# Performance work log

Measured on AMD Instinct MI355X. Metric: run time of the kernel, lower is better.

## Reference

```python
import jax, jax.numpy as jnp
import numpy as np

B, R, CIN, J, O, ITERS = 512, 1152, 8, 10, 16, 3  # batch, routes, in_ch, capsules, out_ch, routing iters


def squash(s, axis):
    # v = (||s||^2 / (1 + ||s||^2)) * s / ||s||  (standard CapsNet squash)
    sq = jnp.sum(s * s, axis=axis, keepdims=True)
    return (sq / (1.0 + sq)) * s * jax.lax.rsqrt(sq + 1e-8)


def setup_inputs() -> dict:
    key = jax.random.key(0)
    k1, k2 = jax.random.split(key)
    x = jax.random.normal(k1, (B, R, CIN), dtype=jnp.float32)
    W = jax.random.normal(k2, (R, J, O, CIN), dtype=jnp.float32)  # param, batch-broadcast
    return {"x": x, "W": W}


def reference(x, W):
    # u_hat[b,r,j,:] = W[r,j] @ x[b,r]   (replaces torch stack/cat broadcasting)
    u_hat = jnp.einsum('rjoc,brc->brjo', W, x)  # [B,R,J,O]
    b_ij = jnp.zeros((x.shape[0], R, J), dtype=x.dtype)
    v = None
    for it in range(ITERS):
        c_ij = jax.nn.softmax(b_ij, axis=2)                 # softmax over capsules j
        s_j = jnp.einsum('brj,brjo->bjo', c_ij, u_hat)      # weighted sum over routes
        v = squash(s_j, axis=-1)                            # [B,J,O]
        if it < ITERS - 1:
            b_ij = b_ij + jnp.einsum('brjo,bjo->brj', u_hat, v)  # agreement
    # torch returns v_j.squeeze(1) with shape [B, J, O, 1]
    return v[..., None]
```

## Files before the change

### kernel.cpp

```cpp
#include <hip/hip_runtime.h>
#include <hip/hip_fp16.h>
#include <cstdint>
#include <cstddef>

#define NB 512
#define NR 1152
#define NC 8
#define NJ 10
#define NO 16
#define NJO 160
#define NRC 36

typedef unsigned int uint32;

union H2U { __half2 h; uint32 u; };

__device__ __forceinline__ uint32 packf16(float a0, float a1) {
    H2U p;
    p.h = __halves2half2(__float2half_rn(a0), __float2half_rn(a1));
    return p.u;
}
__device__ __forceinline__ float2 unpackf16(uint32 w) {
    H2U p; p.u = w;
    return __half22float2(p.h);
}

__device__ __forceinline__ float dot8f(float4 p, float4 q, float4 xa, float4 xb) {
    return p.x * xa.x + p.y * xa.y + p.z * xa.z + p.w * xa.w
         + q.x * xb.x + q.y * xb.y + q.z * xb.z + q.w * xb.w;
}

__global__ __launch_bounds__(256) void xpose_kernel(const float* __restrict__ x,
                                                    float* __restrict__ xT) {
    const int r0 = blockIdx.x * 16;
    const int b0 = blockIdx.y * 64;
    const int t  = threadIdx.x;
    __shared__ float tile[16][65][8];

    for (int i = t; i < 2048; i += 256) {
        int b = i >> 5, r = (i >> 1) & 15, h = i & 1;
        float4 v = *(const float4*)&x[(size_t)(b0 + b) * (NR * NC) + (size_t)(r0 + r) * NC + h * 4];
        *(float4*)&tile[r][b][h * 4] = v;
    }
    __syncthreads();
    for (int i = t; i < 2048; i += 256) {
        int r = i >> 7, b = (i >> 1) & 63, h = i & 1;
        float4 v = *(const float4*)&tile[r][b][h * 4];
        *(float4*)&xT[(size_t)(r0 + r) * (NB * NC) + (size_t)(b0 + b) * NC + h * 4] = v;
    }
}

__global__ __launch_bounds__(320) void uhat_kernel(const float* __restrict__ xT,
                                                   const float* __restrict__ W,
                                                   uint32* __restrict__ u) {
    const int r = blockIdx.x;
    const int t = threadIdx.x;

    __shared__ float Ws[NC][NJO + 4];
    __shared__ float xs[NB][NC];

    for (int i = t; i < NJO * NC; i += 320) {
        Ws[i & 7][i >> 3] = W[(size_t)r * (NJO * NC) + i];
    }
    {
        const float4* xsrc = (const float4*)(xT + (size_t)r * (NB * NC));
        float4* xdst = (float4*)&xs[0][0];
        for (int i = t; i < (NB * NC) / 4; i += 320) xdst[i] = xsrc[i];
    }
    __syncthreads();

    const int ni   = t % 80;
    const int half = t / 80;
    const int g    = ni / 10;
    const int rem  = ni % 10;
    const int qt   = g >> 1;
    const int jh   = g & 1;
    const int j    = jh * 5 + (rem >> 1);
    const int d    = rem & 1;
    const int jo0  = 16 * j + 4 * qt + 2 * d;

    float w0[8], w1[8];
#pragma unroll
    for (int c = 0; c < 8; ++c) {
        w0[c] = Ws[c][jo0];
        w1[c] = Ws[c][jo0 + 1];
    }

    for (int b = half; b < NB; b += 4) {
        const float4* xp = (const float4*)xs[b];
        float4 xa = xp[0], xb = xp[1];
        float a0 = w0[0] * xa.x + w0[1] * xa.y + w0[2] * xa.z + w0[3] * xa.w
                 + w0[4] * xb.x + w0[5] * xb.y + w0[6] * xb.z + w0[7] * xb.w;
        float a1 = w1[0] * xa.x + w1[1] * xa.y + w1[2] * xa.z + w1[3] * xa.w
                 + w1[4] * xb.x + w1[5] * xb.y + w1[6] * xb.z + w1[7] * xb.w;
        u[(size_t)(b * NR + r) * 80 + ni] = packf16(a0, a1);
    }
}

__global__ __launch_bounds__(320) void s0gemm_kernel(const float* __restrict__ x,
                                                     const float* __restrict__ W,
                                                     float* __restrict__ s0p) {
    const int b0 = blockIdx.x * 32;
    const int rc = blockIdx.y;
    const int r0 = rc * 32;
    const int t  = threadIdx.x;

    __shared__ float xs[32][32][8];

    for (int i = t; i < 2048; i += 320) {
        int bloc = i >> 6, rloc = (i >> 1) & 31, h = i & 1;
        float4 v = *(const float4*)&x[(size_t)(b0 + bloc) * (NR * NC) + (size_t)(r0 + rloc) * NC + h * 4];
        *(float4*)&xs[rloc][bloc][h * 4] = v;
    }
    __syncthreads();

    const int jo = t % 160;
    const int bh = t / 160;

    const float* wp = W + (size_t)r0 * (NJO * NC) + (size_t)jo * NC;

    float acc[16];
#pragma unroll
    for (int i = 0; i < 16; ++i) acc[i] = 0.0f;

#pragma unroll 1
    for (int rloc = 0; rloc < 32; ++rloc) {
        const float* wr = wp + (size_t)rloc * (NJO * NC);
        float4 w0 = *(const float4*)wr;
        float4 w1 = *(const float4*)(wr + 4);
#pragma unroll
        for (int bs = 0; bs < 16; ++bs) {
            const float* xp = xs[rloc][bh * 16 + bs];
            float4 xa = *(const float4*)xp;
            float4 xb = *(const float4*)(xp + 4);
            acc[bs] += dot8f(w0, w1, xa, xb);
        }
    }

#pragma unroll
    for (int bs = 0; bs < 16; ++bs) {
        s0p[((size_t)rc * NB + (b0 + bh * 16 + bs)) * NJO + jo] = acc[bs];
    }
}

#define LOADROW(Q0, Q1, Q2, Q3, Q4, ROW)                                      \
    {                                                                         \
        const uint32* p_ = ubase + (size_t)(ROW) * 80;                        \
        Q0 = *(const uint2*)(p_);     Q1 = *(const uint2*)(p_ + 2);           \
        Q2 = *(const uint2*)(p_ + 4); Q3 = *(const uint2*)(p_ + 6);           \
        Q4 = *(const uint2*)(p_ + 8);                                         \
    }

#define PROCESS(Q0, Q1, Q2, Q3, Q4)                                           \
    {                                                                         \
        uint32 ur[10];                                                        \
        ur[0] = Q0.x; ur[1] = Q0.y; ur[2] = Q1.x; ur[3] = Q1.y;               \
        ur[4] = Q2.x; ur[5] = Q2.y; ur[6] = Q3.x; ur[7] = Q3.y;               \
        ur[8] = Q4.x; ur[9] = Q4.y;                                           \
        float cj[5];                                                          \
        {                                                                     \
            float sum = 0.0f;                                                 \
            _Pragma("unroll")                                                 \
            for (int jl = 0; jl < 5; ++jl) {                                  \
                float2 ua = unpackf16(ur[2 * jl]);                            \
                float2 ub = unpackf16(ur[2 * jl + 1]);                        \
                float4 vv = *(const float4*)&vls[vbase + 16 * jl];            \
                float pj = ua.x * vv.x + ua.y * vv.y + ub.x * vv.z + ub.y * vv.w; \
                pj += __shfl_xor(pj, 1);                                      \
                pj += __shfl_xor(pj, 2);                                      \
                float e = __expf(pj);                                         \
                cj[jl] = e;                                                   \
                sum += e;                                                     \
            }                                                                 \
            sum += __shfl_xor(sum, 4);                                        \
            float inv = 1.0f / sum;                                           \
            _Pragma("unroll")                                                 \
            for (int jl = 0; jl < 5; ++jl) cj[jl] *= inv;                     \
        }                                                                     \
        _Pragma("unroll")                                                     \
        for (int jl = 0; jl < 5; ++jl) {                                      \
            float2 ua = unpackf16(ur[2 * jl]);                                \
            float2 ub = unpackf16(ur[2 * jl + 1]);                            \
            acc[4 * jl + 0] += cj[jl] * ua.x;                                 \
            acc[4 * jl + 1] += cj[jl] * ua.y;                                 \
            acc[4 * jl + 2] += cj[jl] * ub.x;                                 \
            acc[4 * jl + 3] += cj[jl] * ub.y;                                 \
        }                                                                     \
    }

__global__ __launch_bounds__(576, 2) void routing_kernel(const uint32* __restrict__ u,
                                                         const float* __restrict__ s0p,
                                                         float* __restrict__ outp) {
    const int b    = blockIdx.x;
    const int t    = threadIdx.x;
    const int w    = t >> 6;
    const int l    = t & 63;
    const int qt   = l & 3;
    const int jh   = (l >> 2) & 1;
    const int mloc = l >> 3;
    const int g    = qt * 2 + jh;

    __shared__ float sl[NJO];
    __shared__ float vls[NJO];
    __shared__ float vaccl[NJO];

    for (int i = t; i < NJO; i += 576) sl[i] = 0.0f;

    if (t < 80) {
        float sx = 0.0f, sy = 0.0f;
#pragma unroll 6
        for (int rc = 0; rc < NRC; ++rc) {
            float2 p = *(const float2*)&s0p[((size_t)rc * NB + b) * NJO + 2 * t];
            sx += p.x; sy += p.y;
        }
        sx *= 0.1f; sy *= 0.1f;
        float sq = sx * sx + sy * sy;
#pragma unroll
        for (int off = 1; off < 8; off <<= 1) sq += __shfl_xor(sq, off, 8);
        float scale = (sq / (1.0f + sq)) * rsqrtf(sq + 1e-8f);
        float vx = sx * scale, vy = sy * scale;
        *(float2*)&vaccl[2 * t] = make_float2(vx, vy);
        *(float2*)&vls[2 * t]   = make_float2(vx, vy);
    }
    __syncthreads();

    const uint32* ubase = u + (size_t)b * (NR * 80) + g * 10;
    const int vbase = jh * 80 + qt * 4;
    const int rbase = w * 128 + mloc;

#pragma unroll 1
    for (int it = 1; it < 3; ++it) {
        float acc[20];
#pragma unroll
        for (int i = 0; i < 20; ++i) acc[i] = 0.0f;

        uint2 qa0, qa1, qa2, qa3, qa4;
        uint2 qb0, qb1, qb2, qb3, qb4;

        LOADROW(qa0, qa1, qa2, qa3, qa4, rbase)

#pragma unroll 1
        for (int c16 = 0; c16 < 16; c16 += 2) {
            LOADROW(qb0, qb1, qb2, qb3, qb4, rbase + (c16 + 1) * 8)
            PROCESS(qa0, qa1, qa2, qa3, qa4)
            if (c16 < 14) {
                LOADROW(qa0, qa1, qa2, qa3, qa4, rbase + (c16 + 2) * 8)
            }
            PROCESS(qb0, qb1, qb2, qb3, qb4)
        }

        float a[12];
        {
            const int bit = (l >> 3) & 1;
#pragma unroll
            for (int i = 0; i < 12; ++i) {
                float lo = acc[i];
                float hi = (i + 12 < 20) ? acc[i + 12] : 0.0f;
                float send = bit ? lo : hi;
                float recv = __shfl_xor(send, 8);
                a[i] = (bit ? hi : lo) + recv;
            }
        }
#pragma unroll
        for (int st = 1; st < 3; ++st) {
            const int h = 12 >> st;
            const int bit = (l >> (3 + st)) & 1;
#pragma unroll
            for (int i = 0; i < 6; ++i) {
                if (i < h) {
                    float send = bit ? a[i] : a[i + h];
                    float recv = __shfl_xor(send, 8 << st);
                    a[i] = (bit ? a[i + h] : a[i]) + recv;
                }
            }
        }
        const int base = 3 * (__brev((uint32)mloc) >> 29);
#pragma unroll
        for (int i = 0; i < 3; ++i) {
            int aidx = base + i;
            if (aidx < 20) {
                int jl = aidx >> 2, e = aidx & 3;
                atomicAdd(&sl[16 * (jh * 5 + jl) + 4 * qt + e], a[i]);
            }
        }
        __syncthreads();

        if (t < 80) {
            float2 sv = *(const float2*)&sl[2 * t];
            float sq = sv.x * sv.x + sv.y * sv.y;
#pragma unroll
            for (int off = 1; off < 8; off <<= 1) sq += __shfl_xor(sq, off, 8);
            float scale = (sq / (1.0f + sq)) * rsqrtf(sq + 1e-8f);
            float vx = sv.x * scale, vy = sv.y * scale;
            if (it == 2) {
                *(float2*)&outp[b * NJO + 2 * t] = make_float2(vx, vy);
            } else {
                float2 va = *(const float2*)&vaccl[2 * t];
                va.x += vx; va.y += vy;
                *(float2*)&vaccl[2 * t] = va;
                *(float2*)&vls[2 * t]   = va;
            }
        }
        __syncthreads();
        if (it < 2) {
            for (int i = t; i < NJO; i += 576) sl[i] = 0.0f;
            __syncthreads();
        }
    }
}

extern "C" void kernel_launch(void* const* d_in, const int* in_sizes, int n_in,
                              void* d_out, int out_size, void* d_ws, size_t ws_size,
                              hipStream_t stream) {
    (void)in_sizes; (void)n_in; (void)out_size; (void)ws_size;

    const float* x = (const float*)d_in[0];
    const float* W = (const float*)d_in[1];
    float* out = (float*)d_out;

    char* ws = (char*)d_ws;
    const size_t XBYTES = (size_t)NR * NB * NC * 4;
    float*  xT  = (float*)ws;
    uint32* u   = (uint32*)(ws + XBYTES);
    float*  s0p = (float*)ws;

    xpose_kernel<<<dim3(NR / 16, NB / 64), 256, 0, stream>>>(x, xT);
    uhat_kernel<<<NR, 320, 0, stream>>>(xT, W, u);
    s0gemm_kernel<<<dim3(16, NRC), 320, 0, stream>>>(x, W, s0p);
    routing_kernel<<<NB, 576, 0, stream>>>(u, s0p, out);
}
```

Before: 240.9 us.

## Fuse s0 GEMM into uhat kernel and add fallback three-pass routing

The s0 partial GEMM is folded into the tail of the uhat kernel: the first 576 blocks reuse their shared memory to compute s0 partials, with a retiled thread mapping that writes float4 stores. This removes one kernel launch and lets s0 work overlap uhat work, but s0p must now live in its own workspace region. When the workspace is too small, a new routing kernel computes the first routing iteration from u_hat with uniform coefficients instead of reading s0p.

```diff
diff --git a/kernel.cpp b/kernel.cpp
--- a/kernel.cpp
+++ b/kernel.cpp
@@ -52,12 +52,16 @@
 
 __global__ __launch_bounds__(320) void uhat_kernel(const float* __restrict__ xT,
                                                    const float* __restrict__ W,
-                                                   uint32* __restrict__ u) {
+                                                   uint32* __restrict__ u,
+                                                   const float* __restrict__ x,
+                                                   float* __restrict__ s0p,
+                                                   int do_s0) {
     const int r = blockIdx.x;
     const int t = threadIdx.x;
 
-    __shared__ float Ws[NC][NJO + 4];
-    __shared__ float xs[NB][NC];
+    __shared__ char shm[32768 + 512];
+    float (*Ws)[NJO + 4] = (float (*)[NJO + 4])shm;
+    float (*xs)[NC]      = (float (*)[NC])(shm + 5248);
 
     for (int i = t; i < NJO * NC; i += 320) {
         Ws[i & 7][i >> 3] = W[(size_t)r * (NJO * NC) + i];
@@ -71,75 +75,84 @@
 
     const int ni   = t % 80;
     const int half = t / 80;
-    const int g    = ni / 10;
-    const int rem  = ni % 10;
-    const int qt   = g >> 1;
-    const int jh   = g & 1;
-    const int j    = jh * 5 + (rem >> 1);
-    const int d    = rem & 1;
-    const int jo0  = 16 * j + 4 * qt + 2 * d;
-
-    float w0[8], w1[8];
-#pragma unroll
-    for (int c = 0; c < 8; ++c) {
-        w0[c] = Ws[c][jo0];
-        w1[c] = Ws[c][jo0 + 1];
-    }
-
-    for (int b = half; b < NB; b += 4) {
-        const float4* xp = (const float4*)xs[b];
-        float4 xa = xp[0], xb = xp[1];
-        float a0 = w0[0] * xa.x + w0[1] * xa.y + w0[2] * xa.z + w0[3] * xa.w
-                 + w0[4] * xb.x + w0[5] * xb.y + w0[6] * xb.z + w0[7] * xb.w;
-        float a1 = w1[0] * xa.x + w1[1] * xa.y + w1[2] * xa.z + w1[3] * xa.w
-                 + w1[4] * xb.x + w1[5] * xb.y + w1[6] * xb.z + w1[7] * xb.w;
-        u[(size_t)(b * NR + r) * 80 + ni] = packf16(a0, a1);
-    }
-}
-
-__global__ __launch_bounds__(320) void s0gemm_kernel(const float* __restrict__ x,
-                                                     const float* __restrict__ W,
-                                                     float* __restrict__ s0p) {
-    const int b0 = blockIdx.x * 32;
-    const int rc = blockIdx.y;
-    const int r0 = rc * 32;
-    const int t  = threadIdx.x;
-
-    __shared__ float xs[32][32][8];
-
-    for (int i = t; i < 2048; i += 320) {
-        int bloc = i >> 6, rloc = (i >> 1) & 31, h = i & 1;
-        float4 v = *(const float4*)&x[(size_t)(b0 + bloc) * (NR * NC) + (size_t)(r0 + rloc) * NC + h * 4];
-        *(float4*)&xs[rloc][bloc][h * 4] = v;
-    }
-    __syncthreads();
-
-    const int jo = t % 160;
-    const int bh = t / 160;
-
-    const float* wp = W + (size_t)r0 * (NJO * NC) + (size_t)jo * NC;
-
-    float acc[16];
-#pragma unroll
-    for (int i = 0; i < 16; ++i) acc[i] = 0.0f;
+    {
+        const int g    = ni / 10;
+        const int rem  = ni % 10;
+        const int qt   = g >> 1;
+        const int jh   = g & 1;
+        const int j    = jh * 5 + (rem >> 1);
+        const int d    = rem & 1;
+        const int jo0  = 16 * j + 4 * qt + 2 * d;
+
+        float w0[8], w1[8];
+#pragma unroll
+        for (int c = 0; c < 8; ++c) {
+            w0[c] = Ws[c][jo0];
+            w1[c] = Ws[c][jo0 + 1];
+        }
+
+        for (int b = half; b < NB; b += 4) {
+            const float4* xp = (const float4*)xs[b];
+            float4 xa = xp[0], xb = xp[1];
+            float a0 = w0[0] * xa.x + w0[1] * xa.y + w0[2] * xa.z + w0[3] * xa.w
+                     + w0[4] * xb.x + w0[5] * xb.y + w0[6] * xb.z + w0[7] * xb.w;
+            float a1 = w1[0] * xa.x + w1[1] * xa.y + w1[2] * xa.z + w1[3] * xa.w
+                     + w1[4] * xb.x + w1[5] * xb.y + w1[6] * xb.z + w1[7] * xb.w;
+            u[(size_t)(b * NR + r) * 80 + ni] = packf16(a0, a1);
+        }
+    }
+
+    if (do_s0 && r < 576) {
+        __syncthreads();
+        float (*xs2)[32][NC] = (float (*)[32][NC])shm;
+
+        const int b0s = (r % 16) * 32;
+        const int rc  = r / 16;
+        const int r0  = rc * 32;
+
+        for (int i = t; i < 2048; i += 320) {
+            int bloc = i >> 6, rloc = (i >> 1) & 31, h = i & 1;
+            float4 v = *(const float4*)&x[(size_t)(b0s + bloc) * (NR * NC) + (size_t)(r0 + rloc) * NC + h * 4];
+            *(float4*)&xs2[rloc][bloc][h * 4] = v;
+        }
+        __syncthreads();
+
+        const int joq = t % 40;
+        const int bq  = t / 40;
+
+        float acc[16];
+#pragma unroll
+        for (int i = 0; i < 16; ++i) acc[i] = 0.0f;
 
 #pragma unroll 1
-    for (int rloc = 0; rloc < 32; ++rloc) {
-        const float* wr = wp + (size_t)rloc * (NJO * NC);
-        float4 w0 = *(const float4*)wr;
-        float4 w1 = *(const float4*)(wr + 4);
-#pragma unroll
-        for (int bs = 0; bs < 16; ++bs) {
-            const float* xp = xs[rloc][bh * 16 + bs];
-            float4 xa = *(const float4*)xp;
-            float4 xb = *(const float4*)(xp + 4);
-            acc[bs] += dot8f(w0, w1, xa, xb);
-        }
-    }
-
-#pragma unroll
-    for (int bs = 0; bs < 16; ++bs) {
-        s0p[((size_t)rc * NB + (b0 + bh * 16 + bs)) * NJO + jo] = acc[bs];
+        for (int rloc = 0; rloc < 32; ++rloc) {
+            const float* wr = W + ((size_t)(r0 + rloc) * NJO + 4 * joq) * NC;
+            float4 w0a = *(const float4*)(wr);
+            float4 w0b = *(const float4*)(wr + 4);
+            float4 w1a = *(const float4*)(wr + 8);
+            float4 w1b = *(const float4*)(wr + 12);
+            float4 w2a = *(const float4*)(wr + 16);
+            float4 w2b = *(const float4*)(wr + 20);
+            float4 w3a = *(const float4*)(wr + 24);
+            float4 w3b = *(const float4*)(wr + 28);
+#pragma unroll
+            for (int bb = 0; bb < 4; ++bb) {
+                const float* xp = xs2[rloc][bq * 4 + bb];
+                float4 xa = *(const float4*)xp;
+                float4 xb = *(const float4*)(xp + 4);
+                acc[4 * bb + 0] += dot8f(w0a, w0b, xa, xb);
+                acc[4 * bb + 1] += dot8f(w1a, w1b, xa, xb);
+                acc[4 * bb + 2] += dot8f(w2a, w2b, xa, xb);
+                acc[4 * bb + 3] += dot8f(w3a, w3b, xa, xb);
+            }
+        }
+
+#pragma unroll
+        for (int bb = 0; bb < 4; ++bb) {
+            float4 st = make_float4(acc[4 * bb + 0], acc[4 * bb + 1],
+                                    acc[4 * bb + 2], acc[4 * bb + 3]);
+            *(float4*)&s0p[((size_t)rc * NB + (b0s + bq * 4 + bb)) * NJO + 4 * joq] = st;
+        }
     }
 }
 
@@ -151,7 +164,154 @@
         Q4 = *(const uint2*)(p_ + 8);                                         \
     }
 
-#define PROCESS(Q0, Q1, Q2, Q3, Q4)                                           \
+#define PROCESS_A(Q0, Q1, Q2, Q3, Q4)                                         \
+    {                                                                         \
+        uint32 ur[10];                                                        \
+        ur[0] = Q0.x; ur[1] = Q0.y; ur[2] = Q1.x; ur[3] = Q1.y;               \
+        ur[4] = Q2.x; ur[5] = Q2.y; ur[6] = Q3.x; ur[7] = Q3.y;               \
+        ur[8] = Q4.x; ur[9] = Q4.y;                                           \
+        float cj[5];                                                          \
+        if (it == 0) {                                                        \
+            _Pragma("unroll")                                                 \
+            for (int jl = 0; jl < 5; ++jl) cj[jl] = 0.1f;                     \
+        } else {                                                              \
+            float sum = 0.0f;                                                 \
+            _Pragma("unroll")                                                 \
+            for (int jl = 0; jl < 5; ++jl) {                                  \
+                float2 ua = unpackf16(ur[2 * jl]);                            \
+                float2 ub = unpackf16(ur[2 * jl + 1]);                        \
+                float4 vv = *(const float4*)&vls[vbase + 16 * jl];            \
+                float pj = ua.x * vv.x + ua.y * vv.y + ub.x * vv.z + ub.y * vv.w; \
+                pj += __shfl_xor(pj, 1);                                      \
+                pj += __shfl_xor(pj, 2);                                      \
+                float e = __expf(pj);                                         \
+                cj[jl] = e;                                                   \
+                sum += e;                                                     \
+            }                                                                 \
+            sum += __shfl_xor(sum, 4);                                        \
+            float inv = 1.0f / sum;                                           \
+            _Pragma("unroll")                                                 \
+            for (int jl = 0; jl < 5; ++jl) cj[jl] *= inv;                     \
+        }                                                                     \
+        _Pragma("unroll")                                                     \
+        for (int jl = 0; jl < 5; ++jl) {                                      \
+            float2 ua = unpackf16(ur[2 * jl]);                                \
+            float2 ub = unpackf16(ur[2 * jl + 1]);                            \
+            acc[4 * jl + 0] += cj[jl] * ua.x;                                 \
+            acc[4 * jl + 1] += cj[jl] * ua.y;                                 \
+            acc[4 * jl + 2] += cj[jl] * ub.x;                                 \
+            acc[4 * jl + 3] += cj[jl] * ub.y;                                 \
+        }                                                                     \
+    }
+
+__global__ __launch_bounds__(576, 2) void routing3_kernel(const uint32* __restrict__ u,
+                                                          float* __restrict__ outp) {
+    const int b    = blockIdx.x;
+    const int t    = threadIdx.x;
+    const int w    = t >> 6;
+    const int l    = t & 63;
+    const int qt   = l & 3;
+    const int jh   = (l >> 2) & 1;
+    const int mloc = l >> 3;
+    const int g    = qt * 2 + jh;
+
+    __shared__ float sl[NJO];
+    __shared__ float vls[NJO];
+    __shared__ float vaccl[NJO];
+
+    for (int i = t; i < NJO; i += 576) sl[i] = 0.0f;
+    __syncthreads();
+
+    const uint32* ubase = u + (size_t)b * (NR * 80) + g * 10;
+    const int vbase = jh * 80 + qt * 4;
+    const int rbase = w * 128 + mloc;
+
+#pragma unroll 1
+    for (int it = 0; it < 3; ++it) {
+        float acc[20];
+#pragma unroll
+        for (int i = 0; i < 20; ++i) acc[i] = 0.0f;
+
+        uint2 qa0, qa1, qa2, qa3, qa4;
+        uint2 qb0, qb1, qb2, qb3, qb4;
+
+        LOADROW(qa0, qa1, qa2, qa3, qa4, rbase)
+
+#pragma unroll 1
+        for (int c16 = 0; c16 < 16; c16 += 2) {
+            LOADROW(qb0, qb1, qb2, qb3, qb4, rbase + (c16 + 1) * 8)
+            PROCESS_A(qa0, qa1, qa2, qa3, qa4)
+            if (c16 < 14) {
+                LOADROW(qa0, qa1, qa2, qa3, qa4, rbase + (c16 + 2) * 8)
+            }
+            PROCESS_A(qb0, qb1, qb2, qb3, qb4)
+        }
+
+        float a[12];
+        {
+            const int bit = (l >> 3) & 1;
+#pragma unroll
+            for (int i = 0; i < 12; ++i) {
+                float lo = acc[i];
+                float hi = (i + 12 < 20) ? acc[i + 12] : 0.0f;
+                float send = bit ? lo : hi;
+                float recv = __shfl_xor(send, 8);
+                a[i] = (bit ? hi : lo) + recv;
+            }
+        }
+#pragma unroll
+        for (int st = 1; st < 3; ++st) {
+            const int h = 12 >> st;
+            const int bit = (l >> (3 + st)) & 1;
+#pragma unroll
+            for (int i = 0; i < 6; ++i) {
+                if (i < h) {
+                    float send = bit ? a[i] : a[i + h];
+                    float recv = __shfl_xor(send, 8 << st);
+                    a[i] = (bit ? a[i + h] : a[i]) + recv;
+                }
+            }
+        }
+        const int base = 3 * (__brev((uint32)mloc) >> 29);
+#pragma unroll
+        for (int i = 0; i < 3; ++i) {
+            int aidx = base + i;
+            if (aidx < 20) {
+                int jl = aidx >> 2, e = aidx & 3;
+                atomicAdd(&sl[16 * (jh * 5 + jl) + 4 * qt + e], a[i]);
+            }
+        }
+        __syncthreads();
+
+        if (t < 80) {
+            float2 sv = *(const float2*)&sl[2 * t];
+            float sq = sv.x * sv.x + sv.y * sv.y;
+#pragma unroll
+            for (int off = 1; off < 8; off <<= 1) sq += __shfl_xor(sq, off, 8);
+            float scale = (sq / (1.0f + sq)) * rsqrtf(sq + 1e-8f);
+            float vx = sv.x * scale, vy = sv.y * scale;
+            if (it == 2) {
+                *(float2*)&outp[b * NJO + 2 * t] = make_float2(vx, vy);
+            } else {
+                float2 va;
+                if (it == 0) va = make_float2(vx, vy);
+                else {
+                    va = *(const float2*)&vaccl[2 * t];
+                    va.x += vx; va.y += vy;
+                }
+                *(float2*)&vaccl[2 * t] = va;
+                *(float2*)&vls[2 * t]   = va;
+            }
+        }
+        __syncthreads();
+        if (it < 2) {
+            for (int i = t; i < NJO; i += 576) sl[i] = 0.0f;
+            __syncthreads();
+        }
+    }
+}
+
+#define PROCESS_B(Q0, Q1, Q2, Q3, Q4)                                         \
     {                                                                         \
         uint32 ur[10];                                                        \
         ur[0] = Q0.x; ur[1] = Q0.y; ur[2] = Q1.x; ur[3] = Q1.y;               \
@@ -188,9 +348,9 @@
         }                                                                     \
     }
 
-__global__ __launch_bounds__(576, 2) void routing_kernel(const uint32* __restrict__ u,
-                                                         const float* __restrict__ s0p,
-                                                         float* __restrict__ outp) {
+__global__ __launch_bounds__(576, 2) void routing2_kernel(const uint32* __restrict__ u,
+                                                          const float* __restrict__ s0p,
+                                                          float* __restrict__ outp) {
     const int b    = blockIdx.x;
     const int t    = threadIdx.x;
     const int w    = t >> 6;
@@ -242,11 +402,11 @@
 #pragma unroll 1
         for (int c16 = 0; c16 < 16; c16 += 2) {
             LOADROW(qb0, qb1, qb2, qb3, qb4, rbase + (c16 + 1) * 8)
-            PROCESS(qa0, qa1, qa2, qa3, qa4)
+            PROCESS_B(qa0, qa1, qa2, qa3, qa4)
             if (c16 < 14) {
                 LOADROW(qa0, qa1, qa2, qa3, qa4, rbase + (c16 + 2) * 8)
             }
-            PROCESS(qb0, qb1, qb2, qb3, qb4)
+            PROCESS_B(qb0, qb1, qb2, qb3, qb4)
         }
 
         float a[12];
@@ -312,20 +472,27 @@
 extern "C" void kernel_launch(void* const* d_in, const int* in_sizes, int n_in,
                               void* d_out, int out_size, void* d_ws, size_t ws_size,
                               hipStream_t stream) {
-    (void)in_sizes; (void)n_in; (void)out_size; (void)ws_size;
+    (void)in_sizes; (void)n_in; (void)out_size;
 
     const float* x = (const float*)d_in[0];
     const float* W = (const float*)d_in[1];
     float* out = (float*)d_out;
 
     char* ws = (char*)d_ws;
-    const size_t XBYTES = (size_t)NR * NB * NC * 4;
+    const size_t XBYTES  = (size_t)NR * NB * NC * 4;
+    const size_t UBYTES  = (size_t)NB * NR * 80 * 4;
+    const size_t S0PBYTES = (size_t)NRC * NB * NJO * 4;
     float*  xT  = (float*)ws;
     uint32* u   = (uint32*)(ws + XBYTES);
-    float*  s0p = (float*)ws;
+    float*  s0p = (float*)(ws + XBYTES + UBYTES);
+
+    const bool room = (ws_size >= XBYTES + UBYTES + S0PBYTES);
 
     xpose_kernel<<<dim3(NR / 16, NB / 64), 256, 0, stream>>>(x, xT);
-    uhat_kernel<<<NR, 320, 0, stream>>>(xT, W, u);
-    s0gemm_kernel<<<dim3(16, NRC), 320, 0, stream>>>(x, W, s0p);
-    routing_kernel<<<NB, 576, 0, stream>>>(u, s0p, out);
-}
+    uhat_kernel<<<NR, 320, 0, stream>>>(xT, W, u, x, s0p, room ? 1 : 0);
+    if (room) {
+        routing2_kernel<<<NB, 576, 0, stream>>>(u, s0p, out);
+    } else {
+        routing3_kernel<<<NB, 576, 0, stream>>>(u, out);
+    }
+}
```

New measurement: 274.1 us. +13.8%, slower.
